# Performance work log

Hardware: AMD Instinct MI355X
Metric: run time of the kernel (lower is better)

The kernel has to match this reference:

```python
import jax, jax.numpy as jnp
import numpy as np


def setup_inputs() -> dict:
    key = jax.random.key(0)
    ks = jax.random.split(key, 7)
    n, dim, h, d = 4096, 512, 8, 64
    return {
        "Q": jax.random.normal(ks[0], (n, dim), dtype=jnp.float32),
        "K": jax.random.normal(ks[1], (n, dim), dtype=jnp.float32),
        "V": jax.random.normal(ks[2], (n, dim), dtype=jnp.float32),
        "Wq": jax.random.uniform(ks[3], (h, dim, d), dtype=jnp.float32),
        "Wk": jax.random.uniform(ks[4], (h, dim, d), dtype=jnp.float32),
        "Wv": jax.random.uniform(ks[5], (h, dim, d), dtype=jnp.float32),
        "Wo": jax.random.uniform(ks[6], (dim, dim), dtype=jnp.float32),
    }


def reference(Q, K, V, Wq, Wk, Wv, Wo):
    # Per-head projections, vectorized over the head axis h.
    q = jnp.einsum("nd,hde->hne", Q, Wq)  # (h, n, d)
    k = jnp.einsum("md,hde->hme", K, Wk)  # (h, N, d)
    v = jnp.einsum("md,hde->hme", V, Wv)  # (h, N, d)
    d_k = Wq.shape[-1]
    scale = jnp.asarray(1.0 / np.sqrt(d_k), dtype=Q.dtype)
    scores = jnp.einsum("hne,hme->hnm", q, k) * scale  # (h, n, N)
    attn = jax.nn.softmax(scores, axis=-1)  # softmax over keys (row dim 1 of 2D input)
    out = jnp.einsum("hnm,hme->hne", attn, v)  # (h, n, d)
    # Concatenate heads along feature dim in head order, then output projection.
    n = Q.shape[0]
    out = jnp.transpose(out, (1, 0, 2)).reshape(n, -1)  # (n, h*d) == (n, dim)
    return out @ Wo
```

## Files before the change

kernel.cpp:

```cpp
#include <hip/hip_runtime.h>


typedef __attribute__((ext_vector_type(8))) short bf16x8;
typedef __attribute__((ext_vector_type(8))) _Float16 f16x8;
typedef __attribute__((ext_vector_type(4))) float f32x4;
typedef unsigned short u16;

static __device__ __forceinline__ u16 f2bf(float f) {
  union { float f; unsigned u; } v; v.f = f;
  unsigned r = v.u + 0x7fffu + ((v.u >> 16) & 1u);
  return (u16)(r >> 16);
}
static __device__ __forceinline__ float bf2f(u16 h) {
  union { unsigned u; float f; } v; v.u = ((unsigned)h) << 16; return v.f;
}
static __device__ __forceinline__ u16 f2h(float f) {
  union { _Float16 h; u16 u; } v; v.h = (_Float16)f; return v.u;
}
static __device__ __forceinline__ unsigned cvt_pk_bf16(float lo, float hi) {
  unsigned r;
  asm("v_cvt_pk_bf16_f32 %0, %1, %2" : "=v"(r) : "v"(lo), "v"(hi));
  return r;
}
static __device__ __forceinline__ float exp2a(float x) {
  float r;
  asm("v_exp_f32 %0, %1" : "=v"(r) : "v"(x));
  return r;
}
static __device__ __forceinline__ void split2(float v0, float v1,
                                              unsigned& hw, unsigned& lw) {
  unsigned h = cvt_pk_bf16(v0, v1);
  float h0 = __uint_as_float(h << 16);
  float h1 = __uint_as_float(h & 0xffff0000u);
  hw = h;
  lw = cvt_pk_bf16(v0 - h0, v1 - h1);
}

#define MAX3(a, b, c) fmaxf(fmaxf(a, b), c)

#define SWZ(row, byteoff) ((((row) * 128) + (byteoff)) ^ (((row) & 7) << 4))

static __device__ __forceinline__ int sigma64(int k) {
  return (k & 3) | (((k >> 5) & 1) << 2) | (((k >> 2) & 3) << 3) | (((k >> 4) & 1) << 5);
}

#define GLOAD16(gp, lp)                                              \
  __builtin_amdgcn_global_load_lds(                                  \
      (const __attribute__((address_space(1))) void*)(gp),           \
      (__attribute__((address_space(3))) void*)(lp), 16, 0, 0)

__global__ __launch_bounds__(256) void prep_weights(const float* __restrict__ Wq,
                                                    const float* __restrict__ Wk,
                                                    const float* __restrict__ Wv,
                                                    const float* __restrict__ Wo,
                                                    u16* __restrict__ Wall_h,
                                                    u16* __restrict__ Wall_l,
                                                    u16* __restrict__ WoTp) {
  int i = blockIdx.x * 256 + threadIdx.x;
  if (i < 786432) {
    int which = i / 262144, rem = i - which * 262144;
    int b = rem >> 15, r2 = rem & 32767;
    int c = r2 >> 9, r = r2 & 511;
    const float* W = which == 0 ? Wq : which == 1 ? Wk : Wv;
    float x = W[(b << 15) + r * 64 + c];
    u16 h = f2bf(x);
    size_t off = (size_t)(which * 8 + b) * 32768 +
                 (size_t)((r >> 5) * 4 + (c >> 4)) * 512 +
                 ((((r & 31) >> 3) * 16) + (c & 15)) * 8 + (r & 7);
    Wall_h[off] = h;
    Wall_l[off] = f2bf(x - bf2f(h));
  } else if (i < 786432 + 262144) {
    int rem = i - 786432;
    int c = rem >> 9, r = rem & 511;
    size_t off = (size_t)(c >> 6) * 32768 +
                 (size_t)((r >> 5) * 4 + ((c >> 4) & 3)) * 512 +
                 ((((r & 31) >> 3) * 16) + (c & 15)) * 8 + (r & 7);
    WoTp[off] = f2bf(Wo[r * 512 + c]);
  }
}

__global__ __launch_bounds__(256) void proj_gemm(const float* __restrict__ Q,
                                                 const float* __restrict__ Kin,
                                                 const float* __restrict__ Vin,
                                                 const u16* __restrict__ Wall_h,
                                                 const u16* __restrict__ Wall_l,
                                                 u16* __restrict__ qh,
                                                 u16* __restrict__ khg,
                                                 u16* __restrict__ vsg) {
  const int n = 4096, K = 512, N = 64;
  int rb = blockIdx.x;
  int which = blockIdx.y >> 3, b = blockIdx.y & 7;
  int wave = threadIdx.x >> 6, lane = threadIdx.x & 63;
  int lr = lane & 15, lg = lane >> 4;
  int row0 = rb * 64 + wave * 16;

  const float* A = which == 0 ? Q : which == 1 ? Kin : Vin;
  const u16* Bh = Wall_h + (size_t)(which * 8 + b) * 32768 + lane * 8;
  const u16* Bl = Wall_l + (size_t)(which * 8 + b) * 32768 + lane * 8;

  const float* Arow = A + (size_t)(row0 + lr) * K + lg * 8;

  union U8 { unsigned w[4]; bf16x8 v; };
  f32x4 acc[4] = {};

  float4 a0 = *(const float4*)(Arow);
  float4 a1 = *(const float4*)(Arow + 4);
  bf16x8 bh[4], bl[4];
#pragma unroll
  for (int ct = 0; ct < 4; ++ct) bh[ct] = *(const bf16x8*)(Bh + ct * 512);
  if (which != 2) {
#pragma unroll
    for (int ct = 0; ct < 4; ++ct) bl[ct] = *(const bf16x8*)(Bl + ct * 512);
  }

#pragma unroll
  for (int ks = 0; ks < 16; ++ks) {
    float4 a0n, a1n;
    bf16x8 bhn[4], bln[4];
    if (ks < 15) {
      a0n = *(const float4*)(Arow + (ks + 1) * 32);
      a1n = *(const float4*)(Arow + (ks + 1) * 32 + 4);
#pragma unroll
      for (int ct = 0; ct < 4; ++ct)
        bhn[ct] = *(const bf16x8*)(Bh + ((ks + 1) * 4 + ct) * 512);
      if (which != 2) {
#pragma unroll
        for (int ct = 0; ct < 4; ++ct)
          bln[ct] = *(const bf16x8*)(Bl + ((ks + 1) * 4 + ct) * 512);
      }
    }
    U8 ah, al;
    split2(a0.x, a0.y, ah.w[0], al.w[0]);
    split2(a0.z, a0.w, ah.w[1], al.w[1]);
    split2(a1.x, a1.y, ah.w[2], al.w[2]);
    split2(a1.z, a1.w, ah.w[3], al.w[3]);
#pragma unroll
    for (int ct = 0; ct < 4; ++ct)
      acc[ct] = __builtin_amdgcn_mfma_f32_16x16x32_bf16(ah.v, bh[ct], acc[ct], 0, 0, 0);
    if (which != 2) {
#pragma unroll
      for (int ct = 0; ct < 4; ++ct) {
        acc[ct] = __builtin_amdgcn_mfma_f32_16x16x32_bf16(al.v, bh[ct], acc[ct], 0, 0, 0);
        acc[ct] = __builtin_amdgcn_mfma_f32_16x16x32_bf16(ah.v, bl[ct], acc[ct], 0, 0, 0);
      }
    }
    if (ks < 15) {
      a0 = a0n; a1 = a1n;
#pragma unroll
      for (int ct = 0; ct < 4; ++ct) bh[ct] = bhn[ct];
      if (which != 2) {
#pragma unroll
        for (int ct = 0; ct < 4; ++ct) bl[ct] = bln[ct];
      }
    }
  }

  const float QSCALE = 0.125f * 1.44269504f;
#pragma unroll
  for (int ct = 0; ct < 4; ++ct)
#pragma unroll
    for (int r = 0; r < 4; ++r) {
      float v = acc[ct][r];
      int row = row0 + lg * 4 + r;
      int col = ct * 16 + lr;
      if (which == 2) {
        size_t byte = ((size_t)b * 64 + (row >> 6)) * 8192 +
                      SWZ(col, 2 * sigma64(row & 63));
        *(u16*)((char*)vsg + byte) = f2bf(v);
      } else if (which == 1) {
        size_t byte = ((size_t)b * 64 + (row >> 6)) * 8192 + SWZ(row & 63, col * 2);
        *(u16*)((char*)khg + byte) = f2h(v);
      } else {
        qh[((size_t)b * n + row) * N + col] = f2h(v * QSCALE);
      }
    }
}

__global__ __launch_bounds__(256, 4) void attn_kernel(const u16* __restrict__ qh,
                                                      const u16* __restrict__ khg,
                                                      const u16* __restrict__ vsg,
                                                      u16* __restrict__ Opart,
                                                      float2* __restrict__ ml) {
  const int n = 4096, d = 64;
  int bid = blockIdx.x;
  int j = bid & 7, w = bid >> 3;
  int grp = j * 4 + (w >> 5);
  int qb = w & 31;
  int h = grp >> 2, part = grp & 3;
  int wave = threadIdx.x >> 6, lane = threadIdx.x & 63;
  int c = lane & 15, g = lane >> 4;

  __shared__ char SB[32768];

  int qrow0 = qb * 128 + wave * 32;
  f16x8 qf[2][2];
#pragma unroll
  for (int b2 = 0; b2 < 2; ++b2)
#pragma unroll
    for (int ks = 0; ks < 2; ++ks) {
      size_t qoff = ((size_t)h * n + qrow0 + b2 * 16 + c) * d + ks * 32 + g * 8;
      qf[b2][ks] = *(const f16x8*)(qh + qoff);
    }

  f32x4 accO[2][4] = {};
  float m[2] = {-INFINITY, -INFINITY}, l[2] = {0.f, 0.f};

  const char* khB = (const char*)khg + ((size_t)h * 64 + part * 16) * 8192;
  const char* vsB = (const char*)vsg + ((size_t)h * 64 + part * 16) * 8192;
  int so = wave * 2048;
  int sg = so + lane * 16;

#define STAGE(tile, buf)                                            \
  do {                                                              \
    const char* kg_ = khB + (size_t)(tile) * 8192 + sg;             \
    const char* vg_ = vsB + (size_t)(tile) * 8192 + sg;             \
    char* kd_ = SB + (buf) * 8192 + so;                             \
    char* vd_ = SB + 16384 + (buf) * 8192 + so;                     \
    GLOAD16(kg_, kd_);                                              \
    GLOAD16(kg_ + 1024, kd_ + 1024);                                \
    GLOAD16(vg_, vd_);                                              \
    GLOAD16(vg_ + 1024, vd_ + 1024);                                \
  } while (0)

  STAGE(0, 0);

  for (int it = 0; it < 16; ++it) {
    int cur = it & 1;
    asm volatile("s_waitcnt vmcnt(0)" ::: "memory");
    __builtin_amdgcn_s_barrier();
    if (it < 15) STAGE(it + 1, cur ^ 1);

    const char* KHb = SB + cur * 8192;
    const char* VSb = SB + 16384 + cur * 8192;

    f32x4 s[2][4] = {};
    __builtin_amdgcn_s_setprio(1);
#pragma unroll
    for (int ct = 0; ct < 4; ++ct) {
      int R = ct * 16 + c;
#pragma unroll
      for (int ks = 0; ks < 2; ++ks) {
        f16x8 kf = *(const f16x8*)(KHb + SWZ(R, ks * 64 + g * 16));
        s[0][ct] = __builtin_amdgcn_mfma_f32_16x16x32_f16(kf, qf[0][ks], s[0][ct], 0, 0, 0);
        s[1][ct] = __builtin_amdgcn_mfma_f32_16x16x32_f16(kf, qf[1][ks], s[1][ct], 0, 0, 0);
      }
    }
    __builtin_amdgcn_s_setprio(0);

    float mxv[2], mn[2], rs[2];
    bool need[2];
#pragma unroll
    for (int b2 = 0; b2 < 2; ++b2) {
      float t0 = MAX3(s[b2][0][0], s[b2][0][1], s[b2][0][2]);
      float t1 = MAX3(s[b2][0][3], s[b2][1][0], s[b2][1][1]);
      float t2 = MAX3(s[b2][1][2], s[b2][1][3], s[b2][2][0]);
      float t3 = MAX3(s[b2][2][1], s[b2][2][2], s[b2][2][3]);
      float t4 = MAX3(s[b2][3][0], s[b2][3][1], s[b2][3][2]);
      mxv[b2] = fmaxf(MAX3(t0, t1, t2), MAX3(t3, t4, s[b2][3][3]));
    }
#pragma unroll
    for (int b2 = 0; b2 < 2; ++b2) mxv[b2] = fmaxf(mxv[b2], __shfl_xor(mxv[b2], 16));
#pragma unroll
    for (int b2 = 0; b2 < 2; ++b2) mxv[b2] = fmaxf(mxv[b2], __shfl_xor(mxv[b2], 32));
#pragma unroll
    for (int b2 = 0; b2 < 2; ++b2) {
      need[b2] = mxv[b2] > m[b2];
      mn[b2] = need[b2] ? mxv[b2] : m[b2];
      float r0 = 0.f, r1 = 0.f;
#pragma unroll
      for (int ct = 0; ct < 4; ++ct) {
        float q0 = exp2a(s[b2][ct][0] - mn[b2]);
        float q1 = exp2a(s[b2][ct][1] - mn[b2]);
        float q2 = exp2a(s[b2][ct][2] - mn[b2]);
        float q3 = exp2a(s[b2][ct][3] - mn[b2]);
        s[b2][ct][0] = q0; s[b2][ct][1] = q1; s[b2][ct][2] = q2; s[b2][ct][3] = q3;
        r0 += q0 + q1; r1 += q2 + q3;
      }
      rs[b2] = r0 + r1;
    }
#pragma unroll
    for (int b2 = 0; b2 < 2; ++b2) rs[b2] += __shfl_xor(rs[b2], 16);
#pragma unroll
    for (int b2 = 0; b2 < 2; ++b2) rs[b2] += __shfl_xor(rs[b2], 32);
#pragma unroll
    for (int b2 = 0; b2 < 2; ++b2) {
      if (__any(need[b2])) {
        float alpha = exp2a(m[b2] - mn[b2]);
        m[b2] = mn[b2];
        l[b2] = l[b2] * alpha + rs[b2];
#pragma unroll
        for (int r = 0; r < 4; ++r) {
          float ar = __shfl(alpha, g * 4 + r);
#pragma unroll
          for (int dt = 0; dt < 4; ++dt) accO[b2][dt][r] *= ar;
        }
      } else {
        l[b2] += rs[b2];
      }
    }

    union { unsigned w[4]; bf16x8 v; } pa[2][2];
#pragma unroll
    for (int b2 = 0; b2 < 2; ++b2)
#pragma unroll
      for (int ks = 0; ks < 2; ++ks) {
        pa[b2][ks].w[0] = cvt_pk_bf16(s[b2][ks][0], s[b2][ks][1]);
        pa[b2][ks].w[1] = cvt_pk_bf16(s[b2][ks][2], s[b2][ks][3]);
        pa[b2][ks].w[2] = cvt_pk_bf16(s[b2][ks + 2][0], s[b2][ks + 2][1]);
        pa[b2][ks].w[3] = cvt_pk_bf16(s[b2][ks + 2][2], s[b2][ks + 2][3]);
      }

    __builtin_amdgcn_s_setprio(1);
#pragma unroll
    for (int dt = 0; dt < 4; ++dt) {
      int R = dt * 16 + c;
#pragma unroll
      for (int ks = 0; ks < 2; ++ks) {
        bf16x8 vf = *(const bf16x8*)(VSb + SWZ(R, ks * 64 + g * 16));
        accO[0][dt] = __builtin_amdgcn_mfma_f32_16x16x32_bf16(pa[0][ks].v, vf, accO[0][dt], 0, 0, 0);
        accO[1][dt] = __builtin_amdgcn_mfma_f32_16x16x32_bf16(pa[1][ks].v, vf, accO[1][dt], 0, 0, 0);
      }
    }
    __builtin_amdgcn_s_setprio(0);
    __builtin_amdgcn_s_barrier();
  }
#undef STAGE

  u16* Ob = Opart + (((size_t)part * 8 + h) * n) * d;
  float2* mlp = ml + ((size_t)part * 8 + h) * n;
#pragma unroll
  for (int b2 = 0; b2 < 2; ++b2) {
#pragma unroll
    for (int r = 0; r < 4; ++r) {
      int row = qrow0 + b2 * 16 + g * 4 + r;
#pragma unroll
      for (int dt = 0; dt < 4; ++dt)
        Ob[(size_t)row * d + dt * 16 + c] = f2bf(accO[b2][dt][r]);
    }
    if (g == 0) mlp[qrow0 + b2 * 16 + c] = make_float2(m[b2], l[b2]);
  }
}

__global__ __launch_bounds__(256) void attn_combine(const u16* __restrict__ Opart,
                                                    const float2* __restrict__ ml,
                                                    u16* __restrict__ att) {
  int tid = blockIdx.x * 256 + threadIdx.x;
  int chunk = tid & 7;
  int h = (tid >> 3) & 7;
  int row = tid >> 6;
  float2 mls[4];
  float mstar = -INFINITY;
#pragma unroll
  for (int p = 0; p < 4; ++p) {
    mls[p] = ml[((size_t)p * 8 + h) * 4096 + row];
    mstar = fmaxf(mstar, mls[p].x);
  }
  float w[4], denom = 0.f;
#pragma unroll
  for (int p = 0; p < 4; ++p) {
    w[p] = exp2a(mls[p].x - mstar);
    denom += mls[p].y * w[p];
  }
  float inv = 1.f / denom;
  float res[8] = {};
#pragma unroll
  for (int p = 0; p < 4; ++p) {
    bf16x8 o = *(const bf16x8*)(Opart + (((size_t)p * 8 + h) * 4096 + row) * 64 + chunk * 8);
    float wp = w[p] * inv;
#pragma unroll
    for (int j = 0; j < 8; ++j) res[j] += bf2f((u16)o[j]) * wp;
  }
  bf16x8 rv;
#pragma unroll
  for (int j = 0; j < 8; ++j) rv[j] = (short)f2bf(res[j]);
  *(bf16x8*)(att + (size_t)row * 512 + h * 64 + chunk * 8) = rv;
}

__global__ __launch_bounds__(256) void final_gemm(const u16* __restrict__ A,
                                                  const u16* __restrict__ BTp,
                                                  float* __restrict__ out,
                                                  int M, int K, int N) {
  int rb = blockIdx.x, cb = blockIdx.y;
  int wave = threadIdx.x >> 6, lane = threadIdx.x & 63;
  int lr = lane & 15, lg = lane >> 4;
  int row0 = rb * 64 + wave * 16;

  const u16* Arow = A + (size_t)(row0 + lr) * K + lg * 8;
  const u16* Bp = BTp + (size_t)cb * 32768 + lane * 8;

  f32x4 acc[4] = {};
  bf16x8 a = *(const bf16x8*)(Arow);
  bf16x8 bfr[4];
#pragma unroll
  for (int ct = 0; ct < 4; ++ct) bfr[ct] = *(const bf16x8*)(Bp + ct * 512);

#pragma unroll
  for (int ks = 0; ks < 16; ++ks) {
    bf16x8 an, bfn[4];
    if (ks < 15) {
      an = *(const bf16x8*)(Arow + (ks + 1) * 32);
#pragma unroll
      for (int ct = 0; ct < 4; ++ct)
        bfn[ct] = *(const bf16x8*)(Bp + ((ks + 1) * 4 + ct) * 512);
    }
#pragma unroll
    for (int ct = 0; ct < 4; ++ct)
      acc[ct] = __builtin_amdgcn_mfma_f32_16x16x32_bf16(a, bfr[ct], acc[ct], 0, 0, 0);
    if (ks < 15) {
      a = an;
#pragma unroll
      for (int ct = 0; ct < 4; ++ct) bfr[ct] = bfn[ct];
    }
  }
#pragma unroll
  for (int ct = 0; ct < 4; ++ct)
#pragma unroll
    for (int r = 0; r < 4; ++r)
      out[(size_t)(row0 + lg * 4 + r) * N + cb * 64 + ct * 16 + lr] = acc[ct][r];
}

extern "C" void kernel_launch(void* const* d_in, const int* in_sizes, int n_in,
                              void* d_out, int out_size, void* d_ws, size_t ws_size,
                              hipStream_t stream) {
  const float* Q = (const float*)d_in[0];
  const float* K = (const float*)d_in[1];
  const float* V = (const float*)d_in[2];
  const float* Wq = (const float*)d_in[3];
  const float* Wk = (const float*)d_in[4];
  const float* Wv = (const float*)d_in[5];
  const float* Wo = (const float*)d_in[6];
  float* out = (float*)d_out;

  const int n = 4096, dim = 512;
  const size_t KB = 1 << 10, MB = 1 << 20;
  char* ws = (char*)d_ws;
  u16* qh     = (u16*)(ws + 0 * MB);
  u16* khg    = (u16*)(ws + 4 * MB);
  u16* vsg    = (u16*)(ws + 8 * MB);
  u16* Opart  = (u16*)(ws + 12 * MB);
  u16* Wall_h = (u16*)(ws + 12 * MB);
  u16* Wall_l = (u16*)(ws + 12 * MB + 1536 * KB);
  float2* ml  = (float2*)(ws + 28 * MB);
  u16* WoTp   = (u16*)(ws + 29 * MB);
  u16* att    = khg;

  prep_weights<<<4096, 256, 0, stream>>>(Wq, Wk, Wv, Wo, Wall_h, Wall_l, WoTp);

  proj_gemm<<<dim3(n / 64, 24), 256, 0, stream>>>(Q, K, V, Wall_h, Wall_l,
                                                  qh, khg, vsg);

  attn_kernel<<<1024, 256, 0, stream>>>(qh, khg, vsg, Opart, ml);
  attn_combine<<<(n * 8 * 8) / 256, 256, 0, stream>>>(Opart, ml, att);

  final_gemm<<<dim3(n / 64, dim / 64), 256, 0, stream>>>(att, WoTp, out, n, dim, dim);
}
```

Measured before the change: 124.2 us.

## Triple-buffer K/V tiles in attention and fuse split-KV combine into output GEMM

The attention kernel moves from double to triple buffering of K/V tiles in shared memory. It prefetches two tiles ahead, waits with a partial vmcnt, and drops the trailing barrier, with occupancy lowered from 4 to 3 blocks per CU. The separate attn_combine kernel is removed. Its softmax-merge of the four split-KV partials now runs inside final_gemm while the A operand is formed, which saves one launch and one write and read of the intermediate buffer. In exchange, final_gemm recomputes the merge weights in every column block and reads four partials per A fragment, so redundant traffic grows by a factor of 8.

```diff
diff --git a/kernel.cpp b/kernel.cpp
--- a/kernel.cpp
+++ b/kernel.cpp
@@ -176,7 +176,7 @@
     }
 }
 
-__global__ __launch_bounds__(256, 4) void attn_kernel(const u16* __restrict__ qh,
+__global__ __launch_bounds__(256, 3) void attn_kernel(const u16* __restrict__ qh,
                                                       const u16* __restrict__ khg,
                                                       const u16* __restrict__ vsg,
                                                       u16* __restrict__ Opart,
@@ -190,7 +190,7 @@
   int wave = threadIdx.x >> 6, lane = threadIdx.x & 63;
   int c = lane & 15, g = lane >> 4;
 
-  __shared__ char SB[32768];
+  __shared__ char SB[49152];
 
   int qrow0 = qb * 128 + wave * 32;
   f16x8 qf[2][2];
@@ -215,7 +215,7 @@
     const char* kg_ = khB + (size_t)(tile) * 8192 + sg;             \
     const char* vg_ = vsB + (size_t)(tile) * 8192 + sg;             \
     char* kd_ = SB + (buf) * 8192 + so;                             \
-    char* vd_ = SB + 16384 + (buf) * 8192 + so;                     \
+    char* vd_ = SB + 24576 + (buf) * 8192 + so;                     \
     GLOAD16(kg_, kd_);                                              \
     GLOAD16(kg_ + 1024, kd_ + 1024);                                \
     GLOAD16(vg_, vd_);                                              \
@@ -223,15 +223,20 @@
   } while (0)
 
   STAGE(0, 0);
+  STAGE(1, 1);
 
   for (int it = 0; it < 16; ++it) {
-    int cur = it & 1;
-    asm volatile("s_waitcnt vmcnt(0)" ::: "memory");
+    int cur = it % 3;
+    if (it < 15) {
+      asm volatile("s_waitcnt vmcnt(4)" ::: "memory");
+    } else {
+      asm volatile("s_waitcnt vmcnt(0)" ::: "memory");
+    }
     __builtin_amdgcn_s_barrier();
-    if (it < 15) STAGE(it + 1, cur ^ 1);
+    if (it < 14) STAGE(it + 2, (it + 2) % 3);
 
     const char* KHb = SB + cur * 8192;
-    const char* VSb = SB + 16384 + cur * 8192;
+    const char* VSb = SB + 24576 + cur * 8192;
 
     f32x4 s[2][4] = {};
     __builtin_amdgcn_s_setprio(1);
@@ -322,7 +327,6 @@
       }
     }
     __builtin_amdgcn_s_setprio(0);
-    __builtin_amdgcn_s_barrier();
   }
 #undef STAGE
 
@@ -341,73 +345,78 @@
   }
 }
 
-__global__ __launch_bounds__(256) void attn_combine(const u16* __restrict__ Opart,
-                                                    const float2* __restrict__ ml,
-                                                    u16* __restrict__ att) {
-  int tid = blockIdx.x * 256 + threadIdx.x;
-  int chunk = tid & 7;
-  int h = (tid >> 3) & 7;
-  int row = tid >> 6;
-  float2 mls[4];
-  float mstar = -INFINITY;
-#pragma unroll
-  for (int p = 0; p < 4; ++p) {
-    mls[p] = ml[((size_t)p * 8 + h) * 4096 + row];
-    mstar = fmaxf(mstar, mls[p].x);
-  }
-  float w[4], denom = 0.f;
-#pragma unroll
-  for (int p = 0; p < 4; ++p) {
-    w[p] = exp2a(mls[p].x - mstar);
-    denom += mls[p].y * w[p];
-  }
-  float inv = 1.f / denom;
-  float res[8] = {};
-#pragma unroll
-  for (int p = 0; p < 4; ++p) {
-    bf16x8 o = *(const bf16x8*)(Opart + (((size_t)p * 8 + h) * 4096 + row) * 64 + chunk * 8);
-    float wp = w[p] * inv;
-#pragma unroll
-    for (int j = 0; j < 8; ++j) res[j] += bf2f((u16)o[j]) * wp;
-  }
-  bf16x8 rv;
-#pragma unroll
-  for (int j = 0; j < 8; ++j) rv[j] = (short)f2bf(res[j]);
-  *(bf16x8*)(att + (size_t)row * 512 + h * 64 + chunk * 8) = rv;
-}
-
-__global__ __launch_bounds__(256) void final_gemm(const u16* __restrict__ A,
+__global__ __launch_bounds__(256) void final_gemm(const u16* __restrict__ Opart,
+                                                  const float2* __restrict__ ml,
                                                   const u16* __restrict__ BTp,
-                                                  float* __restrict__ out,
-                                                  int M, int K, int N) {
+                                                  float* __restrict__ out) {
+  const int n = 4096, N = 512;
   int rb = blockIdx.x, cb = blockIdx.y;
   int wave = threadIdx.x >> 6, lane = threadIdx.x & 63;
   int lr = lane & 15, lg = lane >> 4;
   int row0 = rb * 64 + wave * 16;
-
-  const u16* Arow = A + (size_t)(row0 + lr) * K + lg * 8;
+  int row = row0 + lr;
+
+  float wn[8][4];
+#pragma unroll
+  for (int h = 0; h < 8; ++h) {
+    float2 mls[4];
+    float mstar = -INFINITY;
+#pragma unroll
+    for (int p = 0; p < 4; ++p) {
+      mls[p] = ml[((size_t)p * 8 + h) * n + row];
+      mstar = fmaxf(mstar, mls[p].x);
+    }
+    float wv[4], denom = 0.f;
+#pragma unroll
+    for (int p = 0; p < 4; ++p) {
+      wv[p] = exp2a(mls[p].x - mstar);
+      denom += mls[p].y * wv[p];
+    }
+    float inv = 1.f / denom;
+#pragma unroll
+    for (int p = 0; p < 4; ++p) wn[h][p] = wv[p] * inv;
+  }
+
   const u16* Bp = BTp + (size_t)cb * 32768 + lane * 8;
 
   f32x4 acc[4] = {};
-  bf16x8 a = *(const bf16x8*)(Arow);
-  bf16x8 bfr[4];
+  bf16x8 o[4], bfr[4];
+#pragma unroll
+  for (int p = 0; p < 4; ++p)
+    o[p] = *(const bf16x8*)(Opart + (((size_t)p * 8 + 0) * n + row) * 64 + lg * 8);
 #pragma unroll
   for (int ct = 0; ct < 4; ++ct) bfr[ct] = *(const bf16x8*)(Bp + ct * 512);
 
 #pragma unroll
   for (int ks = 0; ks < 16; ++ks) {
-    bf16x8 an, bfn[4];
+    int h = ks >> 1;
+    bf16x8 on[4], bfn[4];
     if (ks < 15) {
-      an = *(const bf16x8*)(Arow + (ks + 1) * 32);
+      int hn = (ks + 1) >> 1, halfn = (ks + 1) & 1;
+#pragma unroll
+      for (int p = 0; p < 4; ++p)
+        on[p] = *(const bf16x8*)(Opart + (((size_t)p * 8 + hn) * n + row) * 64 +
+                                 halfn * 32 + lg * 8);
 #pragma unroll
       for (int ct = 0; ct < 4; ++ct)
         bfn[ct] = *(const bf16x8*)(Bp + ((ks + 1) * 4 + ct) * 512);
     }
+    float res[8];
+#pragma unroll
+    for (int jj = 0; jj < 8; ++jj)
+      res[jj] = bf2f((u16)o[0][jj]) * wn[h][0] + bf2f((u16)o[1][jj]) * wn[h][1] +
+                bf2f((u16)o[2][jj]) * wn[h][2] + bf2f((u16)o[3][jj]) * wn[h][3];
+    union { unsigned w[4]; bf16x8 v; } av;
+    av.w[0] = cvt_pk_bf16(res[0], res[1]);
+    av.w[1] = cvt_pk_bf16(res[2], res[3]);
+    av.w[2] = cvt_pk_bf16(res[4], res[5]);
+    av.w[3] = cvt_pk_bf16(res[6], res[7]);
 #pragma unroll
     for (int ct = 0; ct < 4; ++ct)
-      acc[ct] = __builtin_amdgcn_mfma_f32_16x16x32_bf16(a, bfr[ct], acc[ct], 0, 0, 0);
+      acc[ct] = __builtin_amdgcn_mfma_f32_16x16x32_bf16(av.v, bfr[ct], acc[ct], 0, 0, 0);
     if (ks < 15) {
-      a = an;
+#pragma unroll
+      for (int p = 0; p < 4; ++p) o[p] = on[p];
 #pragma unroll
       for (int ct = 0; ct < 4; ++ct) bfr[ct] = bfn[ct];
     }
@@ -442,7 +451,6 @@
   u16* Wall_l = (u16*)(ws + 12 * MB + 1536 * KB);
   float2* ml  = (float2*)(ws + 28 * MB);
   u16* WoTp   = (u16*)(ws + 29 * MB);
-  u16* att    = khg;
 
   prep_weights<<<4096, 256, 0, stream>>>(Wq, Wk, Wv, Wo, Wall_h, Wall_l, WoTp);
 
@@ -450,7 +458,6 @@
                                                   qh, khg, vsg);
 
   attn_kernel<<<1024, 256, 0, stream>>>(qh, khg, vsg, Opart, ml);
-  attn_combine<<<(n * 8 * 8) / 256, 256, 0, stream>>>(Opart, ml, att);
-
-  final_gemm<<<dim3(n / 64, dim / 64), 256, 0, stream>>>(att, WoTp, out, n, dim, dim);
-}
+
+  final_gemm<<<dim3(n / 64, dim / 64), 256, 0, stream>>>(Opart, ml, WoTp, out);
+}
```

Measured after the change: 133.3 us. +7.3%, slower.

## Compute softmax row sums via MFMA with ones, lazy rescale, unroll by two tiles

Applied to the files above, without the earlier changes.

The row-sum reduction in the attention loop is replaced by extra MFMA ops that multiply the bf16 probabilities by a ones matrix, so the sum builds up in an accumulator instead of through VALU adds and cross-lane shuffles. The max rescale is now skipped unless the new max exceeds the old one by more than 8 (a lazy threshold). The loop is unrolled by two with constant buffer indices, and the swizzled LDS offsets are precomputed. This trades a few extra matrix instructions and some exp headroom for less VALU and shuffle work, and the row sum now uses bf16-rounded probabilities.

```diff
diff --git a/kernel.cpp b/kernel.cpp
--- a/kernel.cpp
+++ b/kernel.cpp
@@ -202,128 +202,126 @@
       qf[b2][ks] = *(const f16x8*)(qh + qoff);
     }
 
+  int koff[4][2];
+#pragma unroll
+  for (int ct = 0; ct < 4; ++ct)
+#pragma unroll
+    for (int ks = 0; ks < 2; ++ks)
+      koff[ct][ks] = SWZ(ct * 16 + c, ks * 64 + g * 16);
+
+  union { unsigned w[4]; bf16x8 v; } ones;
+  ones.w[0] = 0x3f803f80u; ones.w[1] = 0x3f803f80u;
+  ones.w[2] = 0x3f803f80u; ones.w[3] = 0x3f803f80u;
+
   f32x4 accO[2][4] = {};
-  float m[2] = {-INFINITY, -INFINITY}, l[2] = {0.f, 0.f};
+  f32x4 accL[2] = {};
+  float m[2] = {-INFINITY, -INFINITY};
 
   const char* khB = (const char*)khg + ((size_t)h * 64 + part * 16) * 8192;
   const char* vsB = (const char*)vsg + ((size_t)h * 64 + part * 16) * 8192;
   int so = wave * 2048;
   int sg = so + lane * 16;
 
-#define STAGE(tile, buf)                                            \
+#define STAGE(tile, BUF)                                            \
   do {                                                              \
     const char* kg_ = khB + (size_t)(tile) * 8192 + sg;             \
     const char* vg_ = vsB + (size_t)(tile) * 8192 + sg;             \
-    char* kd_ = SB + (buf) * 8192 + so;                             \
-    char* vd_ = SB + 16384 + (buf) * 8192 + so;                     \
+    char* kd_ = SB + (BUF)*8192 + so;                               \
+    char* vd_ = SB + 16384 + (BUF)*8192 + so;                       \
     GLOAD16(kg_, kd_);                                              \
     GLOAD16(kg_ + 1024, kd_ + 1024);                                \
     GLOAD16(vg_, vd_);                                              \
     GLOAD16(vg_ + 1024, vd_ + 1024);                                \
   } while (0)
 
+#define TILE(IT, CUR)                                                          \
+  do {                                                                         \
+    asm volatile("s_waitcnt vmcnt(0)" ::: "memory");                           \
+    __builtin_amdgcn_s_barrier();                                              \
+    asm volatile("" ::: "memory");                                             \
+    if ((IT) < 15) STAGE((IT) + 1, 1 - (CUR));                                 \
+    f32x4 s[2][4] = {};                                                        \
+    __builtin_amdgcn_s_setprio(1);                                             \
+    _Pragma("unroll") for (int ct = 0; ct < 4; ++ct) {                         \
+      _Pragma("unroll") for (int ks = 0; ks < 2; ++ks) {                       \
+        f16x8 kf = *(const f16x8*)(SB + (CUR)*8192 + koff[ct][ks]);            \
+        s[0][ct] = __builtin_amdgcn_mfma_f32_16x16x32_f16(kf, qf[0][ks],       \
+                                                          s[0][ct], 0, 0, 0);  \
+        s[1][ct] = __builtin_amdgcn_mfma_f32_16x16x32_f16(kf, qf[1][ks],       \
+                                                          s[1][ct], 0, 0, 0);  \
+      }                                                                        \
+    }                                                                          \
+    __builtin_amdgcn_s_setprio(0);                                             \
+    float mxv[2];                                                              \
+    _Pragma("unroll") for (int b2 = 0; b2 < 2; ++b2) {                         \
+      float t0 = MAX3(s[b2][0][0], s[b2][0][1], s[b2][0][2]);                  \
+      float t1 = MAX3(s[b2][0][3], s[b2][1][0], s[b2][1][1]);                  \
+      float t2 = MAX3(s[b2][1][2], s[b2][1][3], s[b2][2][0]);                  \
+      float t3 = MAX3(s[b2][2][1], s[b2][2][2], s[b2][2][3]);                  \
+      float t4 = MAX3(s[b2][3][0], s[b2][3][1], s[b2][3][2]);                  \
+      mxv[b2] = fmaxf(MAX3(t0, t1, t2), MAX3(t3, t4, s[b2][3][3]));            \
+    }                                                                          \
+    _Pragma("unroll") for (int b2 = 0; b2 < 2; ++b2)                           \
+        mxv[b2] = fmaxf(mxv[b2], __shfl_xor(mxv[b2], 16));                     \
+    _Pragma("unroll") for (int b2 = 0; b2 < 2; ++b2)                           \
+        mxv[b2] = fmaxf(mxv[b2], __shfl_xor(mxv[b2], 32));                     \
+    _Pragma("unroll") for (int b2 = 0; b2 < 2; ++b2) {                         \
+      bool need = mxv[b2] > m[b2] + 8.0f;         \
+      float mn = need ? mxv[b2] : m[b2];                                       \
+      _Pragma("unroll") for (int ct = 0; ct < 4; ++ct) {                       \
+        s[b2][ct][0] = exp2a(s[b2][ct][0] - mn);                               \
+        s[b2][ct][1] = exp2a(s[b2][ct][1] - mn);                               \
+        s[b2][ct][2] = exp2a(s[b2][ct][2] - mn);                               \
+        s[b2][ct][3] = exp2a(s[b2][ct][3] - mn);                               \
+      }                                                                        \
+      if (__any(need)) {                                                       \
+        float alpha = exp2a(m[b2] - mn);                                       \
+        m[b2] = mn;                                                            \
+        _Pragma("unroll") for (int r = 0; r < 4; ++r) {                        \
+          float ar = __shfl(alpha, g * 4 + r);                                 \
+          accL[b2][r] *= ar;                                                   \
+          _Pragma("unroll") for (int dt = 0; dt < 4; ++dt)                     \
+              accO[b2][dt][r] *= ar;                                           \
+        }                                                                      \
+      }                                                                        \
+    }                                                                          \
+    union { unsigned w[4]; bf16x8 v; } pa[2][2];                               \
+    _Pragma("unroll") for (int b2 = 0; b2 < 2; ++b2)                           \
+        _Pragma("unroll") for (int ks = 0; ks < 2; ++ks) {                     \
+      pa[b2][ks].w[0] = cvt_pk_bf16(s[b2][ks][0], s[b2][ks][1]);               \
+      pa[b2][ks].w[1] = cvt_pk_bf16(s[b2][ks][2], s[b2][ks][3]);               \
+      pa[b2][ks].w[2] = cvt_pk_bf16(s[b2][ks + 2][0], s[b2][ks + 2][1]);       \
+      pa[b2][ks].w[3] = cvt_pk_bf16(s[b2][ks + 2][2], s[b2][ks + 2][3]);       \
+    }                                                                          \
+    __builtin_amdgcn_s_setprio(1);                                             \
+    _Pragma("unroll") for (int dt = 0; dt < 4; ++dt) {                         \
+      _Pragma("unroll") for (int ks = 0; ks < 2; ++ks) {                       \
+        bf16x8 vf =                                                            \
+            *(const bf16x8*)(SB + 16384 + (CUR)*8192 + koff[dt][ks]);          \
+        accO[0][dt] = __builtin_amdgcn_mfma_f32_16x16x32_bf16(                 \
+            pa[0][ks].v, vf, accO[0][dt], 0, 0, 0);                            \
+        accO[1][dt] = __builtin_amdgcn_mfma_f32_16x16x32_bf16(                 \
+            pa[1][ks].v, vf, accO[1][dt], 0, 0, 0);                            \
+      }                                                                        \
+    }                                                                          \
+    accL[0] = __builtin_amdgcn_mfma_f32_16x16x32_bf16(pa[0][0].v, ones.v,      \
+                                                      accL[0], 0, 0, 0);       \
+    accL[0] = __builtin_amdgcn_mfma_f32_16x16x32_bf16(pa[0][1].v, ones.v,      \
+                                                      accL[0], 0, 0, 0);       \
+    accL[1] = __builtin_amdgcn_mfma_f32_16x16x32_bf16(pa[1][0].v, ones.v,      \
+                                                      accL[1], 0, 0, 0);       \
+    accL[1] = __builtin_amdgcn_mfma_f32_16x16x32_bf16(pa[1][1].v, ones.v,      \
+                                                      accL[1], 0, 0, 0);       \
+    __builtin_amdgcn_s_setprio(0);                                             \
+  } while (0)
+
   STAGE(0, 0);
-
-  for (int it = 0; it < 16; ++it) {
-    int cur = it & 1;
-    asm volatile("s_waitcnt vmcnt(0)" ::: "memory");
-    __builtin_amdgcn_s_barrier();
-    if (it < 15) STAGE(it + 1, cur ^ 1);
-
-    const char* KHb = SB + cur * 8192;
-    const char* VSb = SB + 16384 + cur * 8192;
-
-    f32x4 s[2][4] = {};
-    __builtin_amdgcn_s_setprio(1);
-#pragma unroll
-    for (int ct = 0; ct < 4; ++ct) {
-      int R = ct * 16 + c;
-#pragma unroll
-      for (int ks = 0; ks < 2; ++ks) {
-        f16x8 kf = *(const f16x8*)(KHb + SWZ(R, ks * 64 + g * 16));
-        s[0][ct] = __builtin_amdgcn_mfma_f32_16x16x32_f16(kf, qf[0][ks], s[0][ct], 0, 0, 0);
-        s[1][ct] = __builtin_amdgcn_mfma_f32_16x16x32_f16(kf, qf[1][ks], s[1][ct], 0, 0, 0);
-      }
-    }
-    __builtin_amdgcn_s_setprio(0);
-
-    float mxv[2], mn[2], rs[2];
-    bool need[2];
-#pragma unroll
-    for (int b2 = 0; b2 < 2; ++b2) {
-      float t0 = MAX3(s[b2][0][0], s[b2][0][1], s[b2][0][2]);
-      float t1 = MAX3(s[b2][0][3], s[b2][1][0], s[b2][1][1]);
-      float t2 = MAX3(s[b2][1][2], s[b2][1][3], s[b2][2][0]);
-      float t3 = MAX3(s[b2][2][1], s[b2][2][2], s[b2][2][3]);
-      float t4 = MAX3(s[b2][3][0], s[b2][3][1], s[b2][3][2]);
-      mxv[b2] = fmaxf(MAX3(t0, t1, t2), MAX3(t3, t4, s[b2][3][3]));
-    }
-#pragma unroll
-    for (int b2 = 0; b2 < 2; ++b2) mxv[b2] = fmaxf(mxv[b2], __shfl_xor(mxv[b2], 16));
-#pragma unroll
-    for (int b2 = 0; b2 < 2; ++b2) mxv[b2] = fmaxf(mxv[b2], __shfl_xor(mxv[b2], 32));
-#pragma unroll
-    for (int b2 = 0; b2 < 2; ++b2) {
-      need[b2] = mxv[b2] > m[b2];
-      mn[b2] = need[b2] ? mxv[b2] : m[b2];
-      float r0 = 0.f, r1 = 0.f;
-#pragma unroll
-      for (int ct = 0; ct < 4; ++ct) {
-        float q0 = exp2a(s[b2][ct][0] - mn[b2]);
-        float q1 = exp2a(s[b2][ct][1] - mn[b2]);
-        float q2 = exp2a(s[b2][ct][2] - mn[b2]);
-        float q3 = exp2a(s[b2][ct][3] - mn[b2]);
-        s[b2][ct][0] = q0; s[b2][ct][1] = q1; s[b2][ct][2] = q2; s[b2][ct][3] = q3;
-        r0 += q0 + q1; r1 += q2 + q3;
-      }
-      rs[b2] = r0 + r1;
-    }
-#pragma unroll
-    for (int b2 = 0; b2 < 2; ++b2) rs[b2] += __shfl_xor(rs[b2], 16);
-#pragma unroll
-    for (int b2 = 0; b2 < 2; ++b2) rs[b2] += __shfl_xor(rs[b2], 32);
-#pragma unroll
-    for (int b2 = 0; b2 < 2; ++b2) {
-      if (__any(need[b2])) {
-        float alpha = exp2a(m[b2] - mn[b2]);
-        m[b2] = mn[b2];
-        l[b2] = l[b2] * alpha + rs[b2];
-#pragma unroll
-        for (int r = 0; r < 4; ++r) {
-          float ar = __shfl(alpha, g * 4 + r);
-#pragma unroll
-          for (int dt = 0; dt < 4; ++dt) accO[b2][dt][r] *= ar;
-        }
-      } else {
-        l[b2] += rs[b2];
-      }
-    }
-
-    union { unsigned w[4]; bf16x8 v; } pa[2][2];
-#pragma unroll
-    for (int b2 = 0; b2 < 2; ++b2)
-#pragma unroll
-      for (int ks = 0; ks < 2; ++ks) {
-        pa[b2][ks].w[0] = cvt_pk_bf16(s[b2][ks][0], s[b2][ks][1]);
-        pa[b2][ks].w[1] = cvt_pk_bf16(s[b2][ks][2], s[b2][ks][3]);
-        pa[b2][ks].w[2] = cvt_pk_bf16(s[b2][ks + 2][0], s[b2][ks + 2][1]);
-        pa[b2][ks].w[3] = cvt_pk_bf16(s[b2][ks + 2][2], s[b2][ks + 2][3]);
-      }
-
-    __builtin_amdgcn_s_setprio(1);
-#pragma unroll
-    for (int dt = 0; dt < 4; ++dt) {
-      int R = dt * 16 + c;
-#pragma unroll
-      for (int ks = 0; ks < 2; ++ks) {
-        bf16x8 vf = *(const bf16x8*)(VSb + SWZ(R, ks * 64 + g * 16));
-        accO[0][dt] = __builtin_amdgcn_mfma_f32_16x16x32_bf16(pa[0][ks].v, vf, accO[0][dt], 0, 0, 0);
-        accO[1][dt] = __builtin_amdgcn_mfma_f32_16x16x32_bf16(pa[1][ks].v, vf, accO[1][dt], 0, 0, 0);
-      }
-    }
-    __builtin_amdgcn_s_setprio(0);
-    __builtin_amdgcn_s_barrier();
-  }
+#pragma unroll 1
+  for (int it2 = 0; it2 < 8; ++it2) {
+    TILE(it2 * 2, 0);
+    TILE(it2 * 2 + 1, 1);
+  }
+#undef TILE
 #undef STAGE
 
   u16* Ob = Opart + (((size_t)part * 8 + h) * n) * d;
@@ -336,8 +334,10 @@
 #pragma unroll
       for (int dt = 0; dt < 4; ++dt)
         Ob[(size_t)row * d + dt * 16 + c] = f2bf(accO[b2][dt][r]);
-    }
-    if (g == 0) mlp[qrow0 + b2 * 16 + c] = make_float2(m[b2], l[b2]);
+      float mrow = __shfl(m[b2], g * 4 + r);
+      if (c == 0)
+        mlp[qrow0 + b2 * 16 + g * 4 + r] = make_float2(mrow, accL[b2][r]);
+    }
   }
 }
 
@@ -368,11 +368,11 @@
     bf16x8 o = *(const bf16x8*)(Opart + (((size_t)p * 8 + h) * 4096 + row) * 64 + chunk * 8);
     float wp = w[p] * inv;
 #pragma unroll
-    for (int j = 0; j < 8; ++j) res[j] += bf2f((u16)o[j]) * wp;
+    for (int jj = 0; jj < 8; ++jj) res[jj] += bf2f((u16)o[jj]) * wp;
   }
   bf16x8 rv;
 #pragma unroll
-  for (int j = 0; j < 8; ++j) rv[j] = (short)f2bf(res[j]);
+  for (int jj = 0; jj < 8; ++jj) rv[jj] = (short)f2bf(res[jj]);
   *(bf16x8*)(att + (size_t)row * 512 + h * 64 + chunk * 8) = rv;
 }
 
```

Measured after the change: 117.8 us. 1.05x faster.
